# Kernel tuning notes

Measured on AMD Instinct MI355X. Metric: run time of the kernel, lower is better.

The kernel has to match this reference:

```python
import jax, jax.numpy as jnp
import numpy as np

B, T, C, H = 256, 256, 512, 64  # batch, seq, n_embd, head_size


def setup_inputs() -> dict:
    key = jax.random.key(0)
    kx, kk, kq, kv = jax.random.split(key, 4)
    x = jax.random.normal(kx, (B, T, C), dtype=jnp.float32)
    # nn.Linear(C, H, bias=False): store as [C, H] so y = x @ W
    Wk = jax.random.normal(kk, (C, H), dtype=jnp.float32) * (C ** -0.5)
    Wq = jax.random.normal(kq, (C, H), dtype=jnp.float32) * (C ** -0.5)
    Wv = jax.random.normal(kv, (C, H), dtype=jnp.float32) * (C ** -0.5)
    return {"x": x, "Wk": Wk, "Wq": Wq, "Wv": Wv}


def reference(x, Wk, Wq, Wv):
    Bx, Tx, Cx = x.shape
    k = jnp.einsum('btc,ch->bth', x, Wk)
    q = jnp.einsum('btc,ch->bth', x, Wq)
    v = jnp.einsum('btc,ch->bth', x, Wv)
    # NOTE: original scales by C**-0.5 (embed dim), not head_size**-0.5
    wei = jnp.einsum('bth,bsh->bts', q, k) * (Cx ** -0.5)  # [B,T,T]
    causal = jnp.tril(jnp.ones((Tx, Tx), dtype=bool))
    wei = jnp.where(causal, wei, -jnp.inf)
    wei = jax.nn.softmax(wei, axis=-1)
    # dropout is identity at inference (deterministic reference)
    out = jnp.einsum('bts,bsh->bth', wei, v)  # [B,T,H]
    return out
```

## Files before the change

### kernel.cpp

```cpp
#include <hip/hip_runtime.h>

#define BB 256
#define TT 256
#define CC 512
#define HH 64

typedef __bf16 bf16;
typedef __bf16 bf16x4 __attribute__((ext_vector_type(4)));
typedef __bf16 bf16x8 __attribute__((ext_vector_type(8)));
typedef float  f32x4  __attribute__((ext_vector_type(4)));

#define MFMA16(a, b, c) __builtin_amdgcn_mfma_f32_16x16x32_bf16((a), (b), (c), 0, 0, 0)

typedef __attribute__((address_space(1))) const void cas1_void;
typedef __attribute__((address_space(3))) void as3_void;
__device__ __forceinline__ void g2lds16(const void* g, void* l) {
    __builtin_amdgcn_global_load_lds((cas1_void*)g, (as3_void*)l, 16, 0, 0);
}

__global__ __launch_bounds__(256) void wtrans(const float* __restrict__ Wk,
                                              const float* __restrict__ Wq,
                                              const float* __restrict__ Wv,
                                              bf16* __restrict__ wt) {
    int which = blockIdx.y;
    const float* W = (which == 0) ? Wq : (which == 1) ? Wk : Wv;
    int idx = blockIdx.x * 256 + threadIdx.x;
    int n = idx & 63, k4 = idx >> 6;
    bf16x4 o;
    #pragma unroll
    for (int i = 0; i < 4; ++i) o[i] = (bf16)W[(k4 * 4 + i) * HH + n];
    *(bf16x4*)(&wt[which * (CC * HH) + n * CC + k4 * 4]) = o;
}

__global__ __launch_bounds__(256, 2) void qkv_gemm(const float* __restrict__ x,
                                                   const bf16* __restrict__ wt,
                                                   bf16* __restrict__ q,
                                                   bf16* __restrict__ k,
                                                   bf16* __restrict__ vt) {
    __shared__ float xs[2][128 * 32];
    __shared__ bf16  wts[2][192 * 32];
    const int tid  = threadIdx.x;
    const int wv   = tid >> 6;
    const int lane = tid & 63;
    const int quad = lane >> 4;
    const int l15  = lane & 15;
    const int l7   = l15 & 7;
    const int l3   = l15 & 3;
    const int rows0 = blockIdx.x * 128;

    auto stage = [&](int p, int kc) {
        #pragma unroll
        for (int j = 0; j < 4; ++j) {
            int s = j * 256 + tid;
            int r = s >> 3, up = s & 7;
            int u = up ^ (r & 7);
            const float* gp = x + (size_t)(rows0 + r) * CC + kc * 32 + u * 4;
            g2lds16(gp, (char*)&xs[p][0] + (j * 256 + wv * 64) * 16);
        }
        #pragma unroll
        for (int j = 0; j < 3; ++j) {
            int n0 = wv * 48 + j * 16;
            int n  = n0 + (lane >> 2);
            int u  = (lane & 3) ^ (n & 3);
            const bf16* gp = wt + (size_t)n * CC + kc * 32 + u * 8;
            g2lds16(gp, (char*)&wts[p][0] + n0 * 64);
        }
    };

    f32x4 acc[2][12];
    #pragma unroll
    for (int mt = 0; mt < 2; ++mt)
        #pragma unroll
        for (int nt = 0; nt < 12; ++nt)
            acc[mt][nt] = (f32x4){0.f, 0.f, 0.f, 0.f};

    stage(0, 0);
    __syncthreads();

    for (int kc = 0; kc < 16; ++kc) {
        int p = kc & 1;
        if (kc < 15) stage(p ^ 1, kc + 1);

        const char* xbase = (const char*)&xs[p][0];
        const char* wbase = (const char*)&wts[p][0];
        #pragma unroll
        for (int mt = 0; mt < 2; ++mt) {
            int row = wv * 32 + mt * 16 + l15;
            const char* rp = xbase + row * 128;
            f32x4 x0 = *(const f32x4*)(rp + (((quad * 2)     ^ l7) * 16));
            f32x4 x1 = *(const f32x4*)(rp + (((quad * 2 + 1) ^ l7) * 16));
            bf16x8 a0;
            #pragma unroll
            for (int j = 0; j < 4; ++j) {
                a0[j] = (bf16)x0[j]; a0[j + 4] = (bf16)x1[j];
            }
            #pragma unroll
            for (int nt = 0; nt < 12; ++nt) {
                int n = (nt >> 2) * 64 + (nt & 3) * 16 + l15;
                const char* np = wbase + n * 64;
                bf16x8 b0 = *(const bf16x8*)(np + ((quad ^ l3) * 16));
                acc[mt][nt] = MFMA16(a0, b0, acc[mt][nt]);
            }
        }
        if (kc < 15) __syncthreads();
    }

    const float scale = 0.044194173824159216f;
    #pragma unroll
    for (int mt = 0; mt < 2; ++mt) {
        int gt = rows0 + wv * 32 + mt * 16 + quad * 4;
        #pragma unroll
        for (int nt = 0; nt < 12; ++nt) {
            int h = (nt & 3) * 16 + l15;
            int wch = nt >> 2;
            if (wch == 0) {
                #pragma unroll
                for (int r = 0; r < 4; ++r)
                    q[(gt + r) * HH + h] = (bf16)(acc[mt][nt][r] * scale);
            } else if (wch == 1) {
                #pragma unroll
                for (int r = 0; r < 4; ++r)
                    k[(gt + r) * HH + h] = (bf16)(acc[mt][nt][r]);
            } else {
                int bb = gt >> 8;
                int tloc = gt & 255;
                bf16x4 pv;
                #pragma unroll
                for (int r = 0; r < 4; ++r) pv[r] = (bf16)(acc[mt][nt][r]);
                *(bf16x4*)(&vt[(bb * HH + h) * TT + tloc]) = pv;
            }
        }
    }
}

__global__ __launch_bounds__(512) void attn(const bf16* __restrict__ q,
                                            const bf16* __restrict__ k,
                                            const bf16* __restrict__ vt,
                                            float* __restrict__ out) {
    __shared__ bf16 ks[256 * 64];
    __shared__ bf16 vs[64 * 256];
    __shared__ bf16 pbuf[8][16 * 264];
    const int tid  = threadIdx.x;
    const int wv   = tid >> 6;
    const int lane = tid & 63;
    const int quad = lane >> 4;
    const int l15  = lane & 15;
    const int b    = blockIdx.x;

    #pragma unroll
    for (int j = 0; j < 4; ++j) {
        int c = wv * 4 + j;
        int s = c * 64 + lane;
        {
            int r = s >> 3, up = s & 7, u = up ^ (r & 7);
            const bf16* gk = k + ((size_t)b * TT + r) * HH + u * 8;
            g2lds16(gk, (char*)ks + c * 1024);
        }
        {
            int r = s >> 5, up = s & 31, u = up ^ (r & 31);
            const bf16* gv = vt + ((size_t)b * HH + r) * TT + u * 8;
            g2lds16(gv, (char*)vs + c * 1024);
        }
    }
    __syncthreads();

    bf16* pb = &pbuf[wv][0];
    const int l7 = l15 & 7;

    #pragma unroll
    for (int ti = 0; ti < 2; ++ti) {
        const int rt = (ti == 0) ? wv : (15 - wv);
        const int rowbase = rt * 16;
        const int ctmax = rt;

        const bf16* qrow = q + ((size_t)b * TT + rowbase + l15) * HH;
        bf16x8 bq0 = *(const bf16x8*)(qrow + quad * 8);
        bf16x8 bq1 = *(const bf16x8*)(qrow + 32 + quad * 8);

        f32x4 sv[16];
        #pragma unroll
        for (int ct = 0; ct < 16; ++ct) {
            if (ct <= ctmax) {
                const char* kp = (const char*)ks + (ct * 16 + l15) * 128;
                bf16x8 k0 = *(const bf16x8*)(kp + ((quad ^ l7) * 16));
                bf16x8 k1 = *(const bf16x8*)(kp + (((4 + quad) ^ l7) * 16));
                f32x4 a = (f32x4){0.f, 0.f, 0.f, 0.f};
                a = MFMA16(k0, bq0, a);
                a = MFMA16(k1, bq1, a);
                int t = rowbase + l15;
                #pragma unroll
                for (int r = 0; r < 4; ++r) {
                    int s = ct * 16 + quad * 4 + r;
                    sv[ct][r] = (s <= t) ? a[r] : -3.0e38f;
                }
            }
        }

        float mx = -3.0e38f;
        #pragma unroll
        for (int ct = 0; ct < 16; ++ct)
            if (ct <= ctmax) {
                #pragma unroll
                for (int r = 0; r < 4; ++r) mx = fmaxf(mx, sv[ct][r]);
            }
        mx = fmaxf(mx, __shfl_xor(mx, 16));
        mx = fmaxf(mx, __shfl_xor(mx, 32));

        float sm = 0.f;
        #pragma unroll
        for (int ct = 0; ct < 16; ++ct) {
            if (ct <= ctmax) {
                bf16x4 ev;
                #pragma unroll
                for (int r = 0; r < 4; ++r) {
                    float e = __expf(sv[ct][r] - mx);
                    sm += e;
                    ev[r] = (bf16)e;
                }
                *(bf16x4*)(&pb[l15 * 264 + ct * 16 + quad * 4]) = ev;
            }
        }
        if (!(ctmax & 1)) {
            int ctz = ctmax + 1;
            *(bf16x4*)(&pb[l15 * 264 + ctz * 16 + quad * 4]) =
                (bf16x4){(bf16)0.f, (bf16)0.f, (bf16)0.f, (bf16)0.f};
        }
        sm += __shfl_xor(sm, 16);
        sm += __shfl_xor(sm, 32);
        asm volatile("" ::: "memory");

        f32x4 o[4];
        #pragma unroll
        for (int ht = 0; ht < 4; ++ht) o[ht] = (f32x4){0.f, 0.f, 0.f, 0.f};
        #pragma unroll
        for (int ks2 = 0; ks2 < 8; ++ks2) {
            if (ks2 <= (ctmax >> 1)) {
                bf16x8 pf = *(const bf16x8*)(&pb[l15 * 264 + ks2 * 32 + quad * 8]);
                #pragma unroll
                for (int ht = 0; ht < 4; ++ht) {
                    int vr = ht * 16 + l15;
                    bf16x8 vf = *(const bf16x8*)((const char*)vs + vr * 512
                                                 + (((ks2 * 4 + quad) ^ (vr & 31)) * 16));
                    o[ht] = MFMA16(vf, pf, o[ht]);
                }
            }
        }

        float rinv = 1.0f / sm;
        int t = rowbase + l15;
        #pragma unroll
        for (int ht = 0; ht < 4; ++ht) {
            f32x4 ov;
            #pragma unroll
            for (int r = 0; r < 4; ++r) ov[r] = o[ht][r] * rinv;
            *(f32x4*)(&out[((size_t)b * TT + t) * HH + ht * 16 + quad * 4]) = ov;
        }
        asm volatile("" ::: "memory");
    }
}

extern "C" void kernel_launch(void* const* d_in, const int* in_sizes, int n_in,
                              void* d_out, int out_size, void* d_ws, size_t ws_size,
                              hipStream_t stream) {
    const float* x  = (const float*)d_in[0];
    const float* Wk = (const float*)d_in[1];
    const float* Wq = (const float*)d_in[2];
    const float* Wv = (const float*)d_in[3];

    bf16* ws = (bf16*)d_ws;
    bf16* wt = ws;
    bf16* q  = ws + 3 * CC * HH;
    bf16* k  = q + (size_t)BB * TT * HH;
    bf16* vt = k + (size_t)BB * TT * HH;
    float* out = (float*)d_out;

    wtrans<<<dim3(32, 3), 256, 0, stream>>>(Wk, Wq, Wv, wt);
    qkv_gemm<<<dim3(512), 256, 0, stream>>>(x, wt, q, k, vt);
    attn<<<dim3(256), 512, 0, stream>>>(q, k, vt, out);
}
```

Measured before the change: 214.8 us.

## Fuse QKV projection and causal attention into one per-batch kernel

Merges the QKV GEMM and attention kernels so each 512-thread block computes Q, K and V^T for one batch element directly into swizzled shared memory, then runs causal attention from LDS. This removes the global-memory round trip of bf16 Q/K/V and one kernel launch. It also splits the P-buffer softmax/PV loop into two halves with a smaller swizzled P buffer so the whole working set fits in 128KB of LDS. The cost is a larger LDS footprint per block and only 256 blocks for the GEMM phase, which lowers occupancy and parallelism compared with the previous 512-block GEMM.

```diff
diff --git a/kernel.cpp b/kernel.cpp
--- a/kernel.cpp
+++ b/kernel.cpp
@@ -32,13 +32,10 @@
     *(bf16x4*)(&wt[which * (CC * HH) + n * CC + k4 * 4]) = o;
 }
 
-__global__ __launch_bounds__(256, 2) void qkv_gemm(const float* __restrict__ x,
-                                                   const bf16* __restrict__ wt,
-                                                   bf16* __restrict__ q,
-                                                   bf16* __restrict__ k,
-                                                   bf16* __restrict__ vt) {
-    __shared__ float xs[2][128 * 32];
-    __shared__ bf16  wts[2][192 * 32];
+__global__ __launch_bounds__(512, 2) void fused(const float* __restrict__ x,
+                                                const bf16* __restrict__ wt,
+                                                float* __restrict__ out) {
+    __shared__ __align__(16) char smem[131072];
     const int tid  = threadIdx.x;
     const int wv   = tid >> 6;
     const int lane = tid & 63;
@@ -46,24 +43,28 @@
     const int l15  = lane & 15;
     const int l7   = l15 & 7;
     const int l3   = l15 & 3;
-    const int rows0 = blockIdx.x * 128;
+    const int b    = blockIdx.x;
+    const float* xg = x + (size_t)b * TT * CC;
 
     auto stage = [&](int p, int kc) {
+        char* xbase = smem + p * 32768;
         #pragma unroll
         for (int j = 0; j < 4; ++j) {
-            int s = j * 256 + tid;
+            int s = j * 512 + tid;
             int r = s >> 3, up = s & 7;
             int u = up ^ (r & 7);
-            const float* gp = x + (size_t)(rows0 + r) * CC + kc * 32 + u * 4;
-            g2lds16(gp, (char*)&xs[p][0] + (j * 256 + wv * 64) * 16);
-        }
-        #pragma unroll
-        for (int j = 0; j < 3; ++j) {
-            int n0 = wv * 48 + j * 16;
-            int n  = n0 + (lane >> 2);
-            int u  = (lane & 3) ^ (n & 3);
-            const bf16* gp = wt + (size_t)n * CC + kc * 32 + u * 8;
-            g2lds16(gp, (char*)&wts[p][0] + n0 * 64);
+            const float* gp = xg + (size_t)r * CC + kc * 32 + u * 4;
+            g2lds16(gp, xbase + (j * 512 + wv * 64) * 16);
+        }
+        if (wv < 6) {
+            char* wbase = smem + 65536 + p * 12288;
+            #pragma unroll
+            for (int j = 0; j < 2; ++j) {
+                int n = wv * 32 + j * 16 + (lane >> 2);
+                int u = (lane & 3) ^ (n & 3);
+                const bf16* gp = wt + (size_t)n * CC + kc * 32 + u * 8;
+                g2lds16(gp, wbase + (wv * 32 + j * 16) * 64);
+            }
         }
     };
 
@@ -81,8 +82,8 @@
         int p = kc & 1;
         if (kc < 15) stage(p ^ 1, kc + 1);
 
-        const char* xbase = (const char*)&xs[p][0];
-        const char* wbase = (const char*)&wts[p][0];
+        const char* xbase = smem + p * 32768;
+        const char* wbase = smem + 65536 + p * 12288;
         #pragma unroll
         for (int mt = 0; mt < 2; ++mt) {
             int row = wv * 32 + mt * 16 + l15;
@@ -102,70 +103,46 @@
                 acc[mt][nt] = MFMA16(a0, b0, acc[mt][nt]);
             }
         }
-        if (kc < 15) __syncthreads();
+        __syncthreads();
     }
 
+    bf16* qs = (bf16*)smem;
+    bf16* ks = (bf16*)(smem + 32768);
+    bf16* vs = (bf16*)(smem + 65536);
     const float scale = 0.044194173824159216f;
     #pragma unroll
     for (int mt = 0; mt < 2; ++mt) {
-        int gt = rows0 + wv * 32 + mt * 16 + quad * 4;
+        int gt = wv * 32 + mt * 16 + quad * 4;
         #pragma unroll
         for (int nt = 0; nt < 12; ++nt) {
             int h = (nt & 3) * 16 + l15;
             int wch = nt >> 2;
             if (wch == 0) {
                 #pragma unroll
-                for (int r = 0; r < 4; ++r)
-                    q[(gt + r) * HH + h] = (bf16)(acc[mt][nt][r] * scale);
+                for (int r = 0; r < 4; ++r) {
+                    int row = gt + r;
+                    *(bf16*)((char*)qs + row * 128 + (((h >> 3) ^ (row & 7)) * 16)
+                             + (h & 7) * 2) = (bf16)(acc[mt][nt][r] * scale);
+                }
             } else if (wch == 1) {
                 #pragma unroll
-                for (int r = 0; r < 4; ++r)
-                    k[(gt + r) * HH + h] = (bf16)(acc[mt][nt][r]);
+                for (int r = 0; r < 4; ++r) {
+                    int row = gt + r;
+                    *(bf16*)((char*)ks + row * 128 + (((h >> 3) ^ (row & 7)) * 16)
+                             + (h & 7) * 2) = (bf16)(acc[mt][nt][r]);
+                }
             } else {
-                int bb = gt >> 8;
-                int tloc = gt & 255;
                 bf16x4 pv;
                 #pragma unroll
                 for (int r = 0; r < 4; ++r) pv[r] = (bf16)(acc[mt][nt][r]);
-                *(bf16x4*)(&vt[(bb * HH + h) * TT + tloc]) = pv;
-            }
-        }
-    }
-}
-
-__global__ __launch_bounds__(512) void attn(const bf16* __restrict__ q,
-                                            const bf16* __restrict__ k,
-                                            const bf16* __restrict__ vt,
-                                            float* __restrict__ out) {
-    __shared__ bf16 ks[256 * 64];
-    __shared__ bf16 vs[64 * 256];
-    __shared__ bf16 pbuf[8][16 * 264];
-    const int tid  = threadIdx.x;
-    const int wv   = tid >> 6;
-    const int lane = tid & 63;
-    const int quad = lane >> 4;
-    const int l15  = lane & 15;
-    const int b    = blockIdx.x;
-
-    #pragma unroll
-    for (int j = 0; j < 4; ++j) {
-        int c = wv * 4 + j;
-        int s = c * 64 + lane;
-        {
-            int r = s >> 3, up = s & 7, u = up ^ (r & 7);
-            const bf16* gk = k + ((size_t)b * TT + r) * HH + u * 8;
-            g2lds16(gk, (char*)ks + c * 1024);
-        }
-        {
-            int r = s >> 5, up = s & 31, u = up ^ (r & 31);
-            const bf16* gv = vt + ((size_t)b * HH + r) * TT + u * 8;
-            g2lds16(gv, (char*)vs + c * 1024);
+                *(bf16x4*)((char*)vs + h * 512 + (((gt >> 3) ^ (h & 31)) * 16)
+                           + ((gt >> 2) & 1) * 8) = pv;
+            }
         }
     }
     __syncthreads();
 
-    bf16* pb = &pbuf[wv][0];
-    const int l7 = l15 & 7;
+    bf16* pb = (bf16*)(smem + 98304 + wv * 4096);
 
     #pragma unroll
     for (int ti = 0; ti < 2; ++ti) {
@@ -173,9 +150,10 @@
         const int rowbase = rt * 16;
         const int ctmax = rt;
 
-        const bf16* qrow = q + ((size_t)b * TT + rowbase + l15) * HH;
-        bf16x8 bq0 = *(const bf16x8*)(qrow + quad * 8);
-        bf16x8 bq1 = *(const bf16x8*)(qrow + 32 + quad * 8);
+        const int qr = rowbase + l15;
+        const char* qp = (const char*)qs + qr * 128;
+        bf16x8 bq0 = *(const bf16x8*)(qp + ((quad ^ l7) * 16));
+        bf16x8 bq1 = *(const bf16x8*)(qp + (((4 + quad) ^ l7) * 16));
 
         f32x4 sv[16];
         #pragma unroll
@@ -207,44 +185,59 @@
         mx = fmaxf(mx, __shfl_xor(mx, 32));
 
         float sm = 0.f;
-        #pragma unroll
-        for (int ct = 0; ct < 16; ++ct) {
-            if (ct <= ctmax) {
-                bf16x4 ev;
-                #pragma unroll
-                for (int r = 0; r < 4; ++r) {
-                    float e = __expf(sv[ct][r] - mx);
-                    sm += e;
-                    ev[r] = (bf16)e;
-                }
-                *(bf16x4*)(&pb[l15 * 264 + ct * 16 + quad * 4]) = ev;
-            }
-        }
-        if (!(ctmax & 1)) {
-            int ctz = ctmax + 1;
-            *(bf16x4*)(&pb[l15 * 264 + ctz * 16 + quad * 4]) =
-                (bf16x4){(bf16)0.f, (bf16)0.f, (bf16)0.f, (bf16)0.f};
+        f32x4 o[4];
+        #pragma unroll
+        for (int ht = 0; ht < 4; ++ht) o[ht] = (f32x4){0.f, 0.f, 0.f, 0.f};
+
+        #pragma unroll
+        for (int hp = 0; hp < 2; ++hp) {
+            if (hp * 8 <= ctmax) {
+                #pragma unroll
+                for (int c2 = 0; c2 < 8; ++c2) {
+                    int ct = hp * 8 + c2;
+                    if (ct <= ctmax) {
+                        bf16x4 ev;
+                        #pragma unroll
+                        for (int r = 0; r < 4; ++r) {
+                            float e = __expf(sv[ct][r] - mx);
+                            sm += e;
+                            ev[r] = (bf16)e;
+                        }
+                        int u = 2 * c2 + (quad >> 1);
+                        *(bf16x4*)((char*)pb + l15 * 256 + ((u ^ l15) * 16)
+                                   + (quad & 1) * 8) = ev;
+                    }
+                }
+                if (ctmax >= hp * 8 && ctmax < hp * 8 + 8 && !(ctmax & 1)) {
+                    int c2z = (ctmax & 7) + 1;
+                    int u = 2 * c2z + (quad >> 1);
+                    *(bf16x4*)((char*)pb + l15 * 256 + ((u ^ l15) * 16)
+                               + (quad & 1) * 8) =
+                        (bf16x4){(bf16)0.f, (bf16)0.f, (bf16)0.f, (bf16)0.f};
+                }
+                asm volatile("" ::: "memory");
+
+                #pragma unroll
+                for (int k2 = 0; k2 < 4; ++k2) {
+                    int ks2 = hp * 4 + k2;
+                    if (ks2 <= (ctmax >> 1)) {
+                        int ur = 4 * k2 + quad;
+                        bf16x8 pf = *(const bf16x8*)((char*)pb + l15 * 256
+                                                     + ((ur ^ l15) * 16));
+                        #pragma unroll
+                        for (int ht = 0; ht < 4; ++ht) {
+                            int vr = ht * 16 + l15;
+                            bf16x8 vf = *(const bf16x8*)((const char*)vs + vr * 512
+                                         + (((ks2 * 4 + quad) ^ (vr & 31)) * 16));
+                            o[ht] = MFMA16(vf, pf, o[ht]);
+                        }
+                    }
+                }
+                asm volatile("" ::: "memory");
+            }
         }
         sm += __shfl_xor(sm, 16);
         sm += __shfl_xor(sm, 32);
-        asm volatile("" ::: "memory");
-
-        f32x4 o[4];
-        #pragma unroll
-        for (int ht = 0; ht < 4; ++ht) o[ht] = (f32x4){0.f, 0.f, 0.f, 0.f};
-        #pragma unroll
-        for (int ks2 = 0; ks2 < 8; ++ks2) {
-            if (ks2 <= (ctmax >> 1)) {
-                bf16x8 pf = *(const bf16x8*)(&pb[l15 * 264 + ks2 * 32 + quad * 8]);
-                #pragma unroll
-                for (int ht = 0; ht < 4; ++ht) {
-                    int vr = ht * 16 + l15;
-                    bf16x8 vf = *(const bf16x8*)((const char*)vs + vr * 512
-                                                 + (((ks2 * 4 + quad) ^ (vr & 31)) * 16));
-                    o[ht] = MFMA16(vf, pf, o[ht]);
-                }
-            }
-        }
 
         float rinv = 1.0f / sm;
         int t = rowbase + l15;
@@ -267,14 +260,9 @@
     const float* Wq = (const float*)d_in[2];
     const float* Wv = (const float*)d_in[3];
 
-    bf16* ws = (bf16*)d_ws;
-    bf16* wt = ws;
-    bf16* q  = ws + 3 * CC * HH;
-    bf16* k  = q + (size_t)BB * TT * HH;
-    bf16* vt = k + (size_t)BB * TT * HH;
+    bf16* wt = (bf16*)d_ws;
     float* out = (float*)d_out;
 
     wtrans<<<dim3(32, 3), 256, 0, stream>>>(Wk, Wq, Wv, wt);
-    qkv_gemm<<<dim3(512), 256, 0, stream>>>(x, wt, q, k, vt);
-    attn<<<dim3(256), 512, 0, stream>>>(q, k, vt, out);
-}
+    fused<<<dim3(256), 512, 0, stream>>>(x, wt, out);
+}
```

Measured after the change: 210.9 us. No clear change (-1.8%).
